# Kernel optimization log

Hardware: AMD Instinct MI355X
Metric: run time of the kernel (lower is better)

The kernel has to match this reference:

```python
import jax, jax.numpy as jnp
import numpy as np

QMIN, QMAX = -128, 127

def make_accurate_lut():
    # lut[i, j] = signed8(j) * signed8(i) with indices taken as uint8 bit patterns
    v = np.arange(256)
    v[v >= 128] -= 256
    xx, yy = np.meshgrid(v, v)
    return jnp.asarray((xx * yy).astype(np.int32))

def setup_inputs() -> dict:
    key = jax.random.key(0)
    kx, kw = jax.random.split(key)
    B, N, M, K = 4, 512, 512, 256
    x = jax.random.normal(kx, (B, N, M), dtype=jnp.float32)
    w = jax.random.normal(kw, (K, M), dtype=jnp.float32)
    return {
        "x": x,
        "w": w,
        "lut": make_accurate_lut(),                       # [256,256] int32
        "x_scale": jnp.ones((1,), jnp.float32) * 0.03,    # per-tensor affine quant params
        "x_zero_point": jnp.zeros((1,), jnp.float32),
        "w_scale": jnp.ones((1,), jnp.float32) * 0.03,
        "w_zero_point": jnp.zeros((1,), jnp.float32),
    }

def _quantize(t, scale, zp):
    # affine quantize to signed int8 range, kept in int32 for indexing
    q = jnp.round(t / scale + zp)
    return jnp.clip(q, QMIN, QMAX).astype(jnp.int32)

def _lut_gemm(xq, wq, lut):
    # xq: [B,N,M] int32 in [-128,127]; wq: [K,M]; lut: [256,256]
    xi = jnp.mod(xq, 256)  # uint8 bit-pattern index
    wi = jnp.mod(wq, 256)
    # gather per-element products via the LUT, then accumulate over M
    prods = lut[xi[:, :, None, :], wi[None, None, :, :]]  # [B,N,K,M] int32
    return prods.sum(axis=-1)                             # [B,N,K] int32

def reference(x, w, lut, x_scale, x_zero_point, w_scale, w_zero_point):
    xs, xzp = x_scale.reshape(()), x_zero_point.reshape(())
    ws, wzp = w_scale.reshape(()), w_zero_point.reshape(())
    M = x.shape[-1]
    xq = _quantize(x, xs, xzp)           # [B,N,M]
    wq = _quantize(w, ws, wzp)           # [K,M]
    acc = _lut_gemm(xq, wq, lut).astype(jnp.float32)  # ~ sum_m xq*wq via LUT
    # affine zero-point correction: sum (xq-xzp)(wq-wzp)
    acc = (acc
           - wzp * jnp.sum(xq, axis=-1, keepdims=True).astype(jnp.float32)
           - xzp * jnp.sum(wq, axis=-1).astype(jnp.float32)[None, None, :]
           + jnp.float32(M) * xzp * wzp)
    return acc * xs * ws                 # dequantized output [B,N,K]
```

## Files before the change

kernel.cpp:

```cpp
#include <hip/hip_runtime.h>

constexpr int Mdim = 512;
constexpr int Kdim = 256;
constexpr int ROWS = 2048;
constexpr int MW   = Mdim / 4;
constexpr int R_PB = 4;

constexpr int XQ_OFF   = 0;
constexpr int WQT_OFF  = 262144;
constexpr int XSUM_OFF = 294912;
constexpr int WSUM_OFF = 296960;

extern "C" __device__ int __ockl_sdot4(int, int, int, bool);
__device__ __forceinline__ int dot4(int a, int b, int c) {
    return __ockl_sdot4(a, b, c, false);
}

__device__ __forceinline__ int qz(float v, float scale, float zp) {
    float q = rintf(v / scale + zp);
    q = fminf(fmaxf(q, -128.0f), 127.0f);
    return (int)q;
}

__device__ __forceinline__ int pack4(int q0, int q1, int q2, int q3) {
    return (q0 & 255) | ((q1 & 255) << 8) | ((q2 & 255) << 16) | ((q3 & 255) << 24);
}

__global__ __launch_bounds__(64) void quant_kernel(
        const float* __restrict__ x, const float* __restrict__ w,
        const float* __restrict__ x_scale, const float* __restrict__ x_zp,
        const float* __restrict__ w_scale, const float* __restrict__ w_zp,
        int* __restrict__ ws) {
    const int tid = threadIdx.x;
    const bool is_x = (blockIdx.x < ROWS);
    const int row = is_x ? blockIdx.x : (blockIdx.x - ROWS);
    const float s  = is_x ? x_scale[0] : w_scale[0];
    const float zp = is_x ? x_zp[0]    : w_zp[0];
    const float* src = (is_x ? x : w) + (size_t)row * Mdim;

    const float4* src4 = (const float4*)src;
    float4 a = src4[tid * 2];
    float4 b = src4[tid * 2 + 1];

    int q0 = qz(a.x, s, zp), q1 = qz(a.y, s, zp), q2 = qz(a.z, s, zp), q3 = qz(a.w, s, zp);
    int q4 = qz(b.x, s, zp), q5 = qz(b.y, s, zp), q6 = qz(b.z, s, zp), q7 = qz(b.w, s, zp);
    int w0 = pack4(q0, q1, q2, q3);
    int w1 = pack4(q4, q5, q6, q7);

    if (is_x) {
        *(int2*)&ws[XQ_OFF + row * MW + 2 * tid] = make_int2(w0, w1);
    } else {
        const int wi0 = 2 * tid;
        const int quad = wi0 >> 2;
        const int sub  = wi0 & 3;
        *(int2*)&ws[WQT_OFF + ((size_t)quad * Kdim + row) * 4 + sub] = make_int2(w0, w1);
    }

    int sum = q0 + q1 + q2 + q3 + q4 + q5 + q6 + q7;
    #pragma unroll
    for (int off = 32; off > 0; off >>= 1) sum += __shfl_down(sum, off);
    if (tid == 0) ws[(is_x ? XSUM_OFF : WSUM_OFF) + row] = sum;
}

__global__ __launch_bounds__(512, 4) void lut_gemm_kernel(
        const int* __restrict__ ws,
        const float* __restrict__ x_scale, const float* __restrict__ x_zp,
        const float* __restrict__ w_scale, const float* __restrict__ w_zp,
        float* __restrict__ out) {
    __shared__ int accs[R_PB][Kdim];

    const int t = threadIdx.x;
    const int k = t & (Kdim - 1);
    const int hu = __builtin_amdgcn_readfirstlane(t >> 8);
    const int r0 = blockIdx.x * R_PB;

    const int4* wq4 = (const int4*)&ws[WQT_OFF];
    int4 wv[16];
    #pragma unroll
    for (int q = 0; q < 16; ++q)
        wv[q] = wq4[(size_t)(hu * 16 + q) * Kdim + k];

    int acc[R_PB];
    #pragma unroll
    for (int r = 0; r < R_PB; ++r) acc[r] = 0;

    const int4* xq4 = (const int4*)&ws[XQ_OFF];
    #pragma unroll
    for (int r = 0; r < R_PB; ++r) {
        const int4* xb = xq4 + (size_t)(r0 + r) * (MW / 4) + hu * 16;
        #pragma unroll
        for (int q = 0; q < 16; ++q) {
            int4 xv = xb[q];
            acc[r] = dot4(xv.x, wv[q].x, acc[r]);
            acc[r] = dot4(xv.y, wv[q].y, acc[r]);
            acc[r] = dot4(xv.z, wv[q].z, acc[r]);
            acc[r] = dot4(xv.w, wv[q].w, acc[r]);
        }
    }

    if (hu == 1) {
        #pragma unroll
        for (int r = 0; r < R_PB; ++r) accs[r][k] = acc[r];
    }
    __syncthreads();
    if (hu == 0) {
        const float xs = x_scale[0], xzpf = x_zp[0];
        const float wsf = w_scale[0], wzpf = w_zp[0];
        const float wsumk = (float)ws[WSUM_OFF + k];
        const float corr_const = (float)Mdim * xzpf * wzpf - xzpf * wsumk;
        const float oscale = xs * wsf;
        #pragma unroll
        for (int r = 0; r < R_PB; ++r) {
            int total = acc[r] + accs[r][k];
            float xsumr = (float)ws[XSUM_OFF + (r0 + r)];
            float v = (float)total - wzpf * xsumr + corr_const;
            out[(size_t)(r0 + r) * Kdim + k] = v * oscale;
        }
    }
}

extern "C" void kernel_launch(void* const* d_in, const int* in_sizes, int n_in,
                              void* d_out, int out_size, void* d_ws, size_t ws_size,
                              hipStream_t stream) {
    const float* x       = (const float*)d_in[0];
    const float* w       = (const float*)d_in[1];
    const float* x_scale = (const float*)d_in[3];
    const float* x_zp    = (const float*)d_in[4];
    const float* w_scale = (const float*)d_in[5];
    const float* w_zp    = (const float*)d_in[6];
    float* out = (float*)d_out;
    int* ws = (int*)d_ws;

    quant_kernel<<<ROWS + Kdim, 64, 0, stream>>>(x, w, x_scale, x_zp, w_scale, w_zp, ws);
    lut_gemm_kernel<<<ROWS / R_PB, 512, 0, stream>>>(ws, x_scale, x_zp, w_scale, w_zp, out);
}
```

Baseline: 75.56 us.

## Replace sdot4 GEMM with int8 MFMA 16x16x64 tiles

Replaces the per-thread sdot4 dot-product GEMM with a matrix-core kernel where each 64-lane wave computes one 16x16 output tile using the i32_16x16x64_i8 MFMA instruction over the full reduction. The quantized weight is stored row-major instead of transposed so both operands load the same way. The goal is to move the integer multiply-accumulate onto matrix cores and cut VALU work. The tradeoffs are a much larger grid of tiny one-wave blocks, no sharing of operands across tiles through LDS, and dependence on the correct MFMA operand and output lane mapping.

```diff
diff --git a/kernel.cpp b/kernel.cpp
--- a/kernel.cpp
+++ b/kernel.cpp
@@ -4,17 +4,13 @@
 constexpr int Kdim = 256;
 constexpr int ROWS = 2048;
 constexpr int MW   = Mdim / 4;
-constexpr int R_PB = 4;
 
 constexpr int XQ_OFF   = 0;
-constexpr int WQT_OFF  = 262144;
-constexpr int XSUM_OFF = 294912;
-constexpr int WSUM_OFF = 296960;
+constexpr int WQ_OFF   = ROWS * MW;
+constexpr int XSUM_OFF = WQ_OFF + Kdim * MW;
+constexpr int WSUM_OFF = XSUM_OFF + ROWS;
 
-extern "C" __device__ int __ockl_sdot4(int, int, int, bool);
-__device__ __forceinline__ int dot4(int a, int b, int c) {
-    return __ockl_sdot4(a, b, c, false);
-}
+typedef int v4i __attribute__((ext_vector_type(4)));
 
 __device__ __forceinline__ int qz(float v, float scale, float zp) {
     float q = rintf(v / scale + zp);
@@ -44,17 +40,9 @@
 
     int q0 = qz(a.x, s, zp), q1 = qz(a.y, s, zp), q2 = qz(a.z, s, zp), q3 = qz(a.w, s, zp);
     int q4 = qz(b.x, s, zp), q5 = qz(b.y, s, zp), q6 = qz(b.z, s, zp), q7 = qz(b.w, s, zp);
-    int w0 = pack4(q0, q1, q2, q3);
-    int w1 = pack4(q4, q5, q6, q7);
 
-    if (is_x) {
-        *(int2*)&ws[XQ_OFF + row * MW + 2 * tid] = make_int2(w0, w1);
-    } else {
-        const int wi0 = 2 * tid;
-        const int quad = wi0 >> 2;
-        const int sub  = wi0 & 3;
-        *(int2*)&ws[WQT_OFF + ((size_t)quad * Kdim + row) * 4 + sub] = make_int2(w0, w1);
-    }
+    const int base = (is_x ? XQ_OFF : WQ_OFF) + row * MW + 2 * tid;
+    *(int2*)&ws[base] = make_int2(pack4(q0, q1, q2, q3), pack4(q4, q5, q6, q7));
 
     int sum = q0 + q1 + q2 + q3 + q4 + q5 + q6 + q7;
     #pragma unroll
@@ -62,60 +50,44 @@
     if (tid == 0) ws[(is_x ? XSUM_OFF : WSUM_OFF) + row] = sum;
 }
 
-__global__ __launch_bounds__(512, 4) void lut_gemm_kernel(
+__global__ __launch_bounds__(64) void mfma_gemm_kernel(
         const int* __restrict__ ws,
         const float* __restrict__ x_scale, const float* __restrict__ x_zp,
         const float* __restrict__ w_scale, const float* __restrict__ w_zp,
         float* __restrict__ out) {
-    __shared__ int accs[R_PB][Kdim];
+    const int lane  = threadIdx.x;
+    const int group = lane >> 4;
+    const int lo    = lane & 15;
+    const int r0 = (blockIdx.x >> 4) * 16;
+    const int c0 = (blockIdx.x & 15) * 16;
 
-    const int t = threadIdx.x;
-    const int k = t & (Kdim - 1);
-    const int hu = __builtin_amdgcn_readfirstlane(t >> 8);
-    const int r0 = blockIdx.x * R_PB;
+    const v4i* xa = (const v4i*)&ws[XQ_OFF + (size_t)(r0 + lo) * MW];
+    const v4i* wb = (const v4i*)&ws[WQ_OFF + (size_t)(c0 + lo) * MW];
 
-    const int4* wq4 = (const int4*)&ws[WQT_OFF];
-    int4 wv[16];
+    v4i a[8], b[8];
     #pragma unroll
-    for (int q = 0; q < 16; ++q)
-        wv[q] = wq4[(size_t)(hu * 16 + q) * Kdim + k];
-
-    int acc[R_PB];
-    #pragma unroll
-    for (int r = 0; r < R_PB; ++r) acc[r] = 0;
-
-    const int4* xq4 = (const int4*)&ws[XQ_OFF];
-    #pragma unroll
-    for (int r = 0; r < R_PB; ++r) {
-        const int4* xb = xq4 + (size_t)(r0 + r) * (MW / 4) + hu * 16;
-        #pragma unroll
-        for (int q = 0; q < 16; ++q) {
-            int4 xv = xb[q];
-            acc[r] = dot4(xv.x, wv[q].x, acc[r]);
-            acc[r] = dot4(xv.y, wv[q].y, acc[r]);
-            acc[r] = dot4(xv.z, wv[q].z, acc[r]);
-            acc[r] = dot4(xv.w, wv[q].w, acc[r]);
-        }
+    for (int kk = 0; kk < 8; ++kk) {
+        a[kk] = xa[kk * 4 + group];
+        b[kk] = wb[kk * 4 + group];
     }
 
-    if (hu == 1) {
-        #pragma unroll
-        for (int r = 0; r < R_PB; ++r) accs[r][k] = acc[r];
-    }
-    __syncthreads();
-    if (hu == 0) {
-        const float xs = x_scale[0], xzpf = x_zp[0];
-        const float wsf = w_scale[0], wzpf = w_zp[0];
-        const float wsumk = (float)ws[WSUM_OFF + k];
-        const float corr_const = (float)Mdim * xzpf * wzpf - xzpf * wsumk;
-        const float oscale = xs * wsf;
-        #pragma unroll
-        for (int r = 0; r < R_PB; ++r) {
-            int total = acc[r] + accs[r][k];
-            float xsumr = (float)ws[XSUM_OFF + (r0 + r)];
-            float v = (float)total - wzpf * xsumr + corr_const;
-            out[(size_t)(r0 + r) * Kdim + k] = v * oscale;
-        }
+    v4i acc = {0, 0, 0, 0};
+    #pragma unroll
+    for (int kk = 0; kk < 8; ++kk)
+        acc = __builtin_amdgcn_mfma_i32_16x16x64_i8(a[kk], b[kk], acc, 0, 0, 0);
+
+    const float xs = x_scale[0], xzpf = x_zp[0];
+    const float wsf = w_scale[0], wzpf = w_zp[0];
+    const float wsumc = (float)ws[WSUM_OFF + c0 + lo];
+    const v4i xs4 = *(const v4i*)&ws[XSUM_OFF + r0 + group * 4];
+    const float corr = (float)Mdim * xzpf * wzpf - xzpf * wsumc;
+    const float oscale = xs * wsf;
+
+    #pragma unroll
+    for (int i = 0; i < 4; ++i) {
+        const int row = r0 + group * 4 + i;
+        float v = (float)acc[i] - wzpf * (float)xs4[i] + corr;
+        out[(size_t)row * Kdim + c0 + lo] = v * oscale;
     }
 }
 
@@ -132,5 +104,6 @@
     int* ws = (int*)d_ws;
 
     quant_kernel<<<ROWS + Kdim, 64, 0, stream>>>(x, w, x_scale, x_zp, w_scale, w_zp, ws);
-    lut_gemm_kernel<<<ROWS / R_PB, 512, 0, stream>>>(ws, x_scale, x_zp, w_scale, w_zp, out);
+    mfma_gemm_kernel<<<(ROWS / 16) * (Kdim / 16), 64, 0, stream>>>(
+        ws, x_scale, x_zp, w_scale, w_zp, out);
 }
```

New measurement: 72.80 us. 3.7% less time.
